# Optimization experiments

Measured on AMD Instinct MI355X. Metric: run time of the kernel, lower is better.

The kernel has to match this reference:

```python
import jax, jax.numpy as jnp
import numpy as np

H = 128
EPS = 1e-5

def _lstm_layer(x, Wih, Whh, bih, bhh):
    # x: [B,T,D] -> h_seq: [B,T,H]. PyTorch gate order: i,f,g,o.
    xw = jnp.einsum('btd,gd->btg', x, Wih) + bih + bhh  # [B,T,4H]
    B = x.shape[0]
    h0 = jnp.zeros((B, H), x.dtype)
    c0 = jnp.zeros((B, H), x.dtype)
    def step(carry, xt):
        h, c = carry
        gates = xt + h @ Whh.T  # [B,4H]
        i, f, g, o = jnp.split(gates, 4, axis=-1)
        i = jax.nn.sigmoid(i); f = jax.nn.sigmoid(f)
        g = jnp.tanh(g); o = jax.nn.sigmoid(o)
        c = f * c + i * g
        h = o * jnp.tanh(c)
        return (h, c), h
    _, hs = jax.lax.scan(step, (h0, c0), jnp.swapaxes(xw, 0, 1))  # [T,B,H]
    return jnp.swapaxes(hs, 0, 1)

def setup_inputs() -> dict:
    key = jax.random.key(0)
    ks = jax.random.split(key, 16)
    B, T, D = 1024, 512, 14
    s = 1.0 / np.sqrt(H)
    u = lambda k, shp: jax.random.uniform(k, shp, jnp.float32, -s, s)
    return {
        'x': jax.random.normal(ks[0], (B, T, D), jnp.float32),
        'Wih0': u(ks[1], (4 * H, D)), 'Whh0': u(ks[2], (4 * H, H)),
        'bih0': u(ks[3], (4 * H,)), 'bhh0': u(ks[4], (4 * H,)),
        'Wih1': u(ks[5], (4 * H, H)), 'Whh1': u(ks[6], (4 * H, H)),
        'bih1': u(ks[7], (4 * H,)), 'bhh1': u(ks[8], (4 * H,)),
        'gamma': jnp.ones((H,), jnp.float32), 'beta': jnp.zeros((H,), jnp.float32),
        'W1': u(ks[9], (32, H)), 'b1': u(ks[10], (32,)),
        'W2': u(ks[11], (1, 32)), 'b2': u(ks[12], (1,)),
    }

def reference(x, Wih0, Whh0, bih0, bhh0, Wih1, Whh1, bih1, bhh1,
              gamma, beta, W1, b1, W2, b2):
    h1 = _lstm_layer(x, Wih0, Whh0, bih0, bhh0)   # [B,T,H] (inter-layer dropout off: eval)
    h2 = _lstm_layer(h1, Wih1, Whh1, bih1, bhh1)  # [B,T,H]
    last = h2[:, -1, :]                            # [B,H]
    mu = jnp.mean(last, axis=0)
    var = jnp.mean((last - mu) ** 2, axis=0)       # biased, matching torch BN
    normalized = (last - mu) / jnp.sqrt(var + EPS) * gamma + beta
    z = jax.nn.relu(normalized @ W1.T + b1)        # dropout identity in eval
    out = z @ W2.T + b2                            # [B,1]
    return out.squeeze(-1)
```

## Files before the change

kernel.cpp:

```cpp
#include <hip/hip_runtime.h>


#define B_ 1024
#define T_ 512
#define D_ 14
#define H_ 128
#define NB 4
#define NT 512

#define L2E 1.44269504088896f
#define L2E2 2.88539008177793f

typedef _Float16 f16;
typedef _Float16 half4 __attribute__((ext_vector_type(4)));
typedef _Float16 half8 __attribute__((ext_vector_type(8)));
typedef _Float16 f16x2 __attribute__((ext_vector_type(2)));
typedef float floatx4 __attribute__((ext_vector_type(4)));

__device__ __forceinline__ float sigmP(float y) {
    return __builtin_amdgcn_rcpf(1.0f + __builtin_amdgcn_exp2f(-y));
}
__device__ __forceinline__ float tanhP(float y) {
    return 1.0f - 2.0f * __builtin_amdgcn_rcpf(1.0f + __builtin_amdgcn_exp2f(y));
}
__device__ __forceinline__ float tanhC(float c) {
    return tanhP(c * L2E2);
}

__device__ __forceinline__ half8 ldfrag_s(const float* __restrict__ p, float s) {
    half8 r;
#pragma unroll
    for (int j = 0; j < 8; ++j) r[j] = (f16)(p[j] * s);
    return r;
}

#define MFMA(a, b, c) __builtin_amdgcn_mfma_f32_16x16x32_f16((a), (b), (c), 0, 0, 0)

__global__ __launch_bounds__(NT, 2) void lstm_fused(
    const float* __restrict__ x,
    const float* __restrict__ Wih0, const float* __restrict__ Whh0,
    const float* __restrict__ bih0, const float* __restrict__ bhh0,
    const float* __restrict__ Wih1, const float* __restrict__ Whh1,
    const float* __restrict__ bih1, const float* __restrict__ bhh1,
    float* __restrict__ h2last)
{
    __shared__ __align__(16) f16 whh1lds[8][4][3][64][8];
    __shared__ __align__(16) f16 h1f[2][4][64][8];
    __shared__ __align__(16) f16 h2f[2][4][64][8];
    __shared__ __align__(16) f16 xf[2][64][8];

    const int tid = threadIdx.x;
    const int lane = tid & 63;
    const int wv = tid >> 6;
    const int n = lane & 15;
    const int q = lane >> 4;
    const int b0 = blockIdx.x * NB;

    {
        unsigned int* z1 = (unsigned int*)h1f;
        unsigned int* z2 = (unsigned int*)h2f;
#pragma unroll
        for (int i = 0; i < 4; ++i) {
            z1[tid + i * 512] = 0u;
            z2[tid + i * 512] = 0u;
        }
        ((unsigned int*)xf)[tid] = 0u;
    }
    __syncthreads();

    if (tid < NB) {
        xf[0][tid + 16][7] = (f16)1.0f;
        xf[1][tid + 16][7] = (f16)1.0f;
    }
    if (tid < 64) {
        int nn = tid & 15, kq = tid >> 4;
        if (nn < NB && kq < 2) {
            half8 v;
#pragma unroll
            for (int e = 0; e < 8; ++e) {
                int k = kq * 8 + e;
                v[e] = (k < D_) ? (f16)x[(size_t)(b0 + nn) * T_ * D_ + k]
                                : (k == 15 ? (f16)1.0f : (f16)0.0f);
            }
            *(half8*)&xf[0][tid][0] = v;
        }
    }

    const float* xpp = x + (size_t)(b0 + (tid & 3)) * T_ * D_ + D_ + (tid >> 2);

    if (wv < 4) {
        half8 aWhh0[2][4][4], aWih0[2][4];
#pragma unroll
        for (int jj = 0; jj < 2; ++jj) {
            const int wg = 2 * wv + jj;
#pragma unroll
            for (int g = 0; g < 4; ++g) {
                const float gs = (g == 2) ? L2E2 : L2E;
                const int gr = g * 128 + wg * 16 + n;
#pragma unroll
                for (int kt = 0; kt < 4; ++kt)
                    aWhh0[jj][g][kt] = ldfrag_s(Whh0 + (size_t)gr * H_ + kt * 32 + q * 8, gs);
                half8 w0;
#pragma unroll
                for (int e = 0; e < 8; ++e) {
                    int k = q * 8 + e;
                    if (k < D_)       w0[e] = (f16)(Wih0[(size_t)gr * D_ + k] * gs);
                    else if (k == 15) w0[e] = (f16)((bih0[gr] + bhh0[gr]) * gs);
                    else              w0[e] = (f16)0.0f;
                }
                aWih0[jj][g] = w0;
            }
        }
        floatx4 c1[2] = {{0.f, 0.f, 0.f, 0.f}, {0.f, 0.f, 0.f, 0.f}};
        __syncthreads();

        for (int p = 0; p <= T_; ++p) {
            const int cur = p & 1, nxt = cur ^ 1;
            if (p < T_) {
                float xp = 0.0f;
                if (tid < NB * D_ && (p + 1) < T_) xp = *xpp;

                floatx4 C0[2][4];
#pragma unroll
                for (int jj = 0; jj < 2; ++jj)
#pragma unroll
                    for (int g = 0; g < 4; ++g) C0[jj][g] = floatx4{0.f, 0.f, 0.f, 0.f};
                {
                    half8 bx = *(const half8*)&xf[cur][lane][0];
#pragma unroll
                    for (int jj = 0; jj < 2; ++jj)
#pragma unroll
                        for (int g = 0; g < 4; ++g) C0[jj][g] = MFMA(aWih0[jj][g], bx, C0[jj][g]);
                }
#pragma unroll
                for (int kt = 0; kt < 4; ++kt) {
                    half8 bh = *(const half8*)&h1f[cur][kt][lane][0];
#pragma unroll
                    for (int jj = 0; jj < 2; ++jj)
#pragma unroll
                        for (int g = 0; g < 4; ++g) C0[jj][g] = MFMA(aWhh0[jj][g][kt], bh, C0[jj][g]);
                }
#pragma unroll
                for (int jj = 0; jj < 2; ++jj) {
                    half4 hp;
#pragma unroll
                    for (int r = 0; r < 4; ++r) {
                        float i_ = sigmP(C0[jj][0][r]);
                        float f_ = sigmP(C0[jj][1][r]);
                        float g_ = tanhP(C0[jj][2][r]);
                        float o_ = sigmP(C0[jj][3][r]);
                        c1[jj][r] = f_ * c1[jj][r] + i_ * g_;
                        hp[r] = (f16)(o_ * tanhC(c1[jj][r]));
                    }
                    const int wg = 2 * wv + jj;
                    const int ktw = wg >> 1;
                    const int qw = (wg & 1) * 2 + (q >> 1);
                    const int eb = (q & 1) * 4;
                    if (n < NB) *(half4*)&h1f[nxt][ktw][n + 16 * qw][eb] = hp;
                }
                if (tid < NB * D_ && (p + 1) < T_) {
                    int k = tid >> 2;
                    xf[nxt][(tid & 3) + 16 * (k >> 3)][k & 7] = (f16)xp;
                    xpp += D_;
                }
            }
            __syncthreads();
        }
    } else {
        const int w = wv - 4;
        half8 aWih1[2][4][4], aWhh1k0[2][4];
        f16x2 b1p[2][4][2];
#pragma unroll
        for (int jj = 0; jj < 2; ++jj) {
            const int wg = 2 * w + jj;
#pragma unroll
            for (int g = 0; g < 4; ++g) {
                const float gs = (g == 2) ? L2E2 : L2E;
                const int gr = g * 128 + wg * 16 + n;
#pragma unroll
                for (int kt = 0; kt < 4; ++kt) {
                    aWih1[jj][g][kt] = ldfrag_s(Wih1 + (size_t)gr * H_ + kt * 32 + q * 8, gs);
                    half8 wf = ldfrag_s(Whh1 + (size_t)gr * H_ + kt * 32 + q * 8, gs);
                    if (kt == 0) aWhh1k0[jj][g] = wf;
                    else         *(half8*)&whh1lds[wg][g][kt - 1][lane][0] = wf;
                }
                const int gb = g * 128 + wg * 16 + q * 4;
                f16x2 p0, p1;
                p0[0] = (f16)((bih1[gb]     + bhh1[gb])     * gs);
                p0[1] = (f16)((bih1[gb + 1] + bhh1[gb + 1]) * gs);
                p1[0] = (f16)((bih1[gb + 2] + bhh1[gb + 2]) * gs);
                p1[1] = (f16)((bih1[gb + 3] + bhh1[gb + 3]) * gs);
                b1p[jj][g][0] = p0;
                b1p[jj][g][1] = p1;
            }
        }
        floatx4 c2[2] = {{0.f, 0.f, 0.f, 0.f}, {0.f, 0.f, 0.f, 0.f}};
        __syncthreads();

        for (int p = 0; p <= T_; ++p) {
            const int cur = p & 1, nxt = cur ^ 1;
            if (p >= 1) {
                floatx4 C1[2][4];
#pragma unroll
                for (int jj = 0; jj < 2; ++jj)
#pragma unroll
                    for (int g = 0; g < 4; ++g) C1[jj][g] = floatx4{0.f, 0.f, 0.f, 0.f};
#pragma unroll
                for (int kt = 0; kt < 4; ++kt) {
                    half8 bh = *(const half8*)&h1f[cur][kt][lane][0];
#pragma unroll
                    for (int jj = 0; jj < 2; ++jj)
#pragma unroll
                        for (int g = 0; g < 4; ++g) C1[jj][g] = MFMA(aWih1[jj][g][kt], bh, C1[jj][g]);
                }
                {
                    half8 bh = *(const half8*)&h2f[cur][0][lane][0];
#pragma unroll
                    for (int jj = 0; jj < 2; ++jj)
#pragma unroll
                        for (int g = 0; g < 4; ++g) C1[jj][g] = MFMA(aWhh1k0[jj][g], bh, C1[jj][g]);
                }
#pragma unroll
                for (int kt = 1; kt < 4; ++kt) {
                    half8 bh = *(const half8*)&h2f[cur][kt][lane][0];
#pragma unroll
                    for (int jj = 0; jj < 2; ++jj) {
                        const int wg = 2 * w + jj;
#pragma unroll
                        for (int g = 0; g < 4; ++g) {
                            half8 aw = *(const half8*)&whh1lds[wg][g][kt - 1][lane][0];
                            C1[jj][g] = MFMA(aw, bh, C1[jj][g]);
                        }
                    }
                }
#pragma unroll
                for (int jj = 0; jj < 2; ++jj) {
                    half4 hp;
                    floatx4 hv;
#pragma unroll
                    for (int r = 0; r < 4; ++r) {
                        float pi = C1[jj][0][r] + (float)b1p[jj][0][r >> 1][r & 1];
                        float pf = C1[jj][1][r] + (float)b1p[jj][1][r >> 1][r & 1];
                        float pg = C1[jj][2][r] + (float)b1p[jj][2][r >> 1][r & 1];
                        float po = C1[jj][3][r] + (float)b1p[jj][3][r >> 1][r & 1];
                        float i_ = sigmP(pi), f_ = sigmP(pf), g_ = tanhP(pg), o_ = sigmP(po);
                        c2[jj][r] = f_ * c2[jj][r] + i_ * g_;
                        hv[r] = o_ * tanhC(c2[jj][r]);
                        hp[r] = (f16)hv[r];
                    }
                    const int wg = 2 * w + jj;
                    const int ktw = wg >> 1;
                    const int qw = (wg & 1) * 2 + (q >> 1);
                    const int eb = (q & 1) * 4;
                    if (n < NB) {
                        *(half4*)&h2f[nxt][ktw][n + 16 * qw][eb] = hp;
                        if (p == T_) {
#pragma unroll
                            for (int r = 0; r < 4; ++r)
                                h2last[(size_t)(b0 + n) * H_ + wg * 16 + q * 4 + r] = hv[r];
                        }
                    }
                }
            }
            __syncthreads();
        }
    }
}

__global__ void bn_stats(const float* __restrict__ h2last, float* __restrict__ stats)
{
    __shared__ float red[2][8][128];
    const int tid = threadIdx.x;
    const int j = tid & 127, bs = tid >> 7;
    float s = 0.0f, ss = 0.0f;
    for (int bb = 0; bb < 128; ++bb) {
        float v = h2last[(size_t)(bb * 8 + bs) * H_ + j];
        s += v;
        ss += v * v;
    }
    red[0][bs][j] = s;
    red[1][bs][j] = ss;
    __syncthreads();
    if (tid < 128) {
        float S = 0.0f, SS = 0.0f;
#pragma unroll
        for (int k = 0; k < 8; ++k) { S += red[0][k][tid]; SS += red[1][k][tid]; }
        float mu = S * (1.0f / 1024.0f);
        float var = SS * (1.0f / 1024.0f) - mu * mu;
        stats[tid] = mu;
        stats[128 + tid] = __builtin_amdgcn_rsqf(var + 1e-5f);
    }
}

__global__ void bn_mlp(const float* __restrict__ h2last, const float* __restrict__ stats,
                       const float* __restrict__ gamma, const float* __restrict__ beta,
                       const float* __restrict__ W1, const float* __restrict__ b1,
                       const float* __restrict__ W2, const float* __restrict__ b2,
                       float* __restrict__ out)
{
    __shared__ float W1T[128][33];
    __shared__ float mus[128], isds[128], gs[128], bts[128], w2s[32];
    const int tid = threadIdx.x;
    const int b = blockIdx.x * 128 + tid;

    for (int i = tid; i < 4096; i += 128) {
        int k = i >> 7, j = i & 127;
        W1T[j][k] = W1[i];
    }
    mus[tid] = stats[tid];
    isds[tid] = stats[128 + tid];
    gs[tid] = gamma[tid];
    bts[tid] = beta[tid];
    if (tid < 32) w2s[tid] = W2[tid];
    __syncthreads();

    float z[32];
#pragma unroll
    for (int k = 0; k < 32; ++k) z[k] = b1[k];

    for (int j = 0; j < 128; ++j) {
        float nv = (h2last[(size_t)b * H_ + j] - mus[j]) * isds[j] * gs[j] + bts[j];
#pragma unroll
        for (int k = 0; k < 32; ++k) z[k] += W1T[j][k] * nv;
    }
    float o = b2[0];
#pragma unroll
    for (int k = 0; k < 32; ++k) o += w2s[k] * fmaxf(z[k], 0.0f);
    out[b] = o;
}

extern "C" void kernel_launch(void* const* d_in, const int* in_sizes, int n_in,
                              void* d_out, int out_size, void* d_ws, size_t ws_size,
                              hipStream_t stream)
{
    const float* x    = (const float*)d_in[0];
    const float* Wih0 = (const float*)d_in[1];
    const float* Whh0 = (const float*)d_in[2];
    const float* bih0 = (const float*)d_in[3];
    const float* bhh0 = (const float*)d_in[4];
    const float* Wih1 = (const float*)d_in[5];
    const float* Whh1 = (const float*)d_in[6];
    const float* bih1 = (const float*)d_in[7];
    const float* bhh1 = (const float*)d_in[8];
    const float* gamma = (const float*)d_in[9];
    const float* beta  = (const float*)d_in[10];
    const float* W1 = (const float*)d_in[11];
    const float* b1 = (const float*)d_in[12];
    const float* W2 = (const float*)d_in[13];
    const float* b2 = (const float*)d_in[14];

    float* h2last = (float*)d_ws;
    float* stats  = h2last + (size_t)B_ * H_;
    float* out = (float*)d_out;

    hipLaunchKernelGGL(lstm_fused, dim3(B_ / NB), dim3(NT), 0, stream,
                       x, Wih0, Whh0, bih0, bhh0, Wih1, Whh1, bih1, bhh1, h2last);
    hipLaunchKernelGGL(bn_stats, dim3(1), dim3(1024), 0, stream, h2last, stats);
    hipLaunchKernelGGL(bn_mlp, dim3(8), dim3(128), 0, stream,
                       h2last, stats, gamma, beta, W1, b1, W2, b2, out);
}
```

Before: 1.117 ms.

## Unify layer-0/layer-1 warps per gate tile and fuse LSTM cell math

Replaces the split where waves 0-3 ran layer 0 and waves 4-7 ran layer 1, each owning two gate tiles. Now every wave owns one 16-row gate tile of both layers and runs both layer steps, so each h1 fragment read from shared memory feeds both layers' MFMAs. More Whh1 fragments stay in registers and the LDS copy shrinks. The cell update is rewritten as one fused routine with five exp2 and two reciprocals in place of separate sigmoid and tanh calls. The cost is higher register pressure per wave, and the changed reciprocal algebra may lose some accuracy.

```diff
diff --git a/kernel.cpp b/kernel.cpp
--- a/kernel.cpp
+++ b/kernel.cpp
@@ -17,16 +17,6 @@
 typedef _Float16 f16x2 __attribute__((ext_vector_type(2)));
 typedef float floatx4 __attribute__((ext_vector_type(4)));
 
-__device__ __forceinline__ float sigmP(float y) {
-    return __builtin_amdgcn_rcpf(1.0f + __builtin_amdgcn_exp2f(-y));
-}
-__device__ __forceinline__ float tanhP(float y) {
-    return 1.0f - 2.0f * __builtin_amdgcn_rcpf(1.0f + __builtin_amdgcn_exp2f(y));
-}
-__device__ __forceinline__ float tanhC(float c) {
-    return tanhP(c * L2E2);
-}
-
 __device__ __forceinline__ half8 ldfrag_s(const float* __restrict__ p, float s) {
     half8 r;
 #pragma unroll
@@ -35,6 +25,24 @@
 }
 
 #define MFMA(a, b, c) __builtin_amdgcn_mfma_f32_16x16x32_f16((a), (b), (c), 0, 0, 0)
+
+__device__ __forceinline__ float cellP(float pi, float pf, float pg, float po, float& cs)
+{
+    float a = __builtin_amdgcn_exp2f(-pi);
+    float u = __builtin_amdgcn_exp2f(-pf);
+    float b = __builtin_amdgcn_exp2f(pg);
+    float d = __builtin_amdgcn_exp2f(-po);
+    float t1 = 1.0f + a;
+    float t3 = 1.0f + u;
+    float t2 = __builtin_fmaf(t1, b, t1);
+    float bm = b - 1.0f;
+    float num = __builtin_fmaf(L2E2 * bm, t3, cs * t2);
+    cs = num * __builtin_amdgcn_rcpf(t2 * t3);
+    float e = __builtin_amdgcn_exp2f(cs);
+    float t4 = 1.0f + d;
+    float t5 = __builtin_fmaf(t4, e, t4);
+    return (e - 1.0f) * __builtin_amdgcn_rcpf(t5);
+}
 
 __global__ __launch_bounds__(NT, 2) void lstm_fused(
     const float* __restrict__ x,
@@ -44,7 +52,7 @@
     const float* __restrict__ bih1, const float* __restrict__ bhh1,
     float* __restrict__ h2last)
 {
-    __shared__ __align__(16) f16 whh1lds[8][4][3][64][8];
+    __shared__ __align__(16) f16 whh1lds[8][4][2][64][8];
     __shared__ __align__(16) f16 h1f[2][4][64][8];
     __shared__ __align__(16) f16 h2f[2][4][64][8];
     __shared__ __align__(16) f16 xf[2][64][8];
@@ -88,182 +96,139 @@
 
     const float* xpp = x + (size_t)(b0 + (tid & 3)) * T_ * D_ + D_ + (tid >> 2);
 
-    if (wv < 4) {
-        half8 aWhh0[2][4][4], aWih0[2][4];
-#pragma unroll
-        for (int jj = 0; jj < 2; ++jj) {
-            const int wg = 2 * wv + jj;
-#pragma unroll
-            for (int g = 0; g < 4; ++g) {
-                const float gs = (g == 2) ? L2E2 : L2E;
-                const int gr = g * 128 + wg * 16 + n;
-#pragma unroll
-                for (int kt = 0; kt < 4; ++kt)
-                    aWhh0[jj][g][kt] = ldfrag_s(Whh0 + (size_t)gr * H_ + kt * 32 + q * 8, gs);
-                half8 w0;
-#pragma unroll
-                for (int e = 0; e < 8; ++e) {
-                    int k = q * 8 + e;
-                    if (k < D_)       w0[e] = (f16)(Wih0[(size_t)gr * D_ + k] * gs);
-                    else if (k == 15) w0[e] = (f16)((bih0[gr] + bhh0[gr]) * gs);
-                    else              w0[e] = (f16)0.0f;
+    const int wg = wv;
+    half8 aWhh0[4][4], aWih0[4];
+    half8 aWih1[4][4], aWhh1r[4][2];
+    f16x2 b1p[4][2];
+#pragma unroll
+    for (int g = 0; g < 4; ++g) {
+        const float gs = (g == 2) ? L2E2 : L2E;
+        const int gr = g * 128 + wg * 16 + n;
+#pragma unroll
+        for (int kt = 0; kt < 4; ++kt)
+            aWhh0[g][kt] = ldfrag_s(Whh0 + (size_t)gr * H_ + kt * 32 + q * 8, gs);
+        half8 w0;
+#pragma unroll
+        for (int e = 0; e < 8; ++e) {
+            int k = q * 8 + e;
+            if (k < D_)       w0[e] = (f16)(Wih0[(size_t)gr * D_ + k] * gs);
+            else if (k == 15) w0[e] = (f16)((bih0[gr] + bhh0[gr]) * gs);
+            else              w0[e] = (f16)0.0f;
+        }
+        aWih0[g] = w0;
+#pragma unroll
+        for (int kt = 0; kt < 4; ++kt) {
+            aWih1[g][kt] = ldfrag_s(Wih1 + (size_t)gr * H_ + kt * 32 + q * 8, gs);
+            half8 wf = ldfrag_s(Whh1 + (size_t)gr * H_ + kt * 32 + q * 8, gs);
+            if (kt < 2) aWhh1r[g][kt] = wf;
+            else        *(half8*)&whh1lds[wg][g][kt - 2][lane][0] = wf;
+        }
+        const int gb = g * 128 + wg * 16 + q * 4;
+        f16x2 p0, p1;
+        p0[0] = (f16)((bih1[gb]     + bhh1[gb])     * gs);
+        p0[1] = (f16)((bih1[gb + 1] + bhh1[gb + 1]) * gs);
+        p1[0] = (f16)((bih1[gb + 2] + bhh1[gb + 2]) * gs);
+        p1[1] = (f16)((bih1[gb + 3] + bhh1[gb + 3]) * gs);
+        b1p[g][0] = p0;
+        b1p[g][1] = p1;
+    }
+
+    floatx4 cs1 = {0.f, 0.f, 0.f, 0.f};
+    floatx4 cs2 = {0.f, 0.f, 0.f, 0.f};
+    __syncthreads();
+
+    for (int p = 0; p <= T_; ++p) {
+        const int cur = p & 1, nxt = cur ^ 1;
+        const bool doA = (p < T_);
+        const bool doB = (p >= 1);
+
+        float xp = 0.0f;
+        if (tid < NB * D_ && (p + 1) < T_) xp = *xpp;
+
+        floatx4 C0[4], C1[4];
+#pragma unroll
+        for (int g = 0; g < 4; ++g) {
+            C0[g] = floatx4{0.f, 0.f, 0.f, 0.f};
+            C1[g] = floatx4{0.f, 0.f, 0.f, 0.f};
+        }
+
+        if (doA) {
+            half8 bx = *(const half8*)&xf[cur][lane][0];
+#pragma unroll
+            for (int g = 0; g < 4; ++g) C0[g] = MFMA(aWih0[g], bx, C0[g]);
+        }
+#pragma unroll
+        for (int kt = 0; kt < 4; ++kt) {
+            half8 bh = *(const half8*)&h1f[cur][kt][lane][0];
+            if (doA) {
+#pragma unroll
+                for (int g = 0; g < 4; ++g) C0[g] = MFMA(aWhh0[g][kt], bh, C0[g]);
+            }
+            if (doB) {
+#pragma unroll
+                for (int g = 0; g < 4; ++g) C1[g] = MFMA(aWih1[g][kt], bh, C1[g]);
+            }
+        }
+        if (doB) {
+#pragma unroll
+            for (int kt = 0; kt < 2; ++kt) {
+                half8 bh = *(const half8*)&h2f[cur][kt][lane][0];
+#pragma unroll
+                for (int g = 0; g < 4; ++g) C1[g] = MFMA(aWhh1r[g][kt], bh, C1[g]);
+            }
+#pragma unroll
+            for (int kt = 2; kt < 4; ++kt) {
+                half8 bh = *(const half8*)&h2f[cur][kt][lane][0];
+#pragma unroll
+                for (int g = 0; g < 4; ++g) {
+                    half8 aw = *(const half8*)&whh1lds[wg][g][kt - 2][lane][0];
+                    C1[g] = MFMA(aw, bh, C1[g]);
                 }
-                aWih0[jj][g] = w0;
-            }
-        }
-        floatx4 c1[2] = {{0.f, 0.f, 0.f, 0.f}, {0.f, 0.f, 0.f, 0.f}};
+            }
+        }
+
+        const int ktw = wg >> 1;
+        const int qw = (wg & 1) * 2 + (q >> 1);
+        const int eb = (q & 1) * 4;
+        if (doA) {
+            half4 hp;
+#pragma unroll
+            for (int r = 0; r < 4; ++r) {
+                float c = cs1[r];
+                hp[r] = (f16)cellP(C0[0][r], C0[1][r], C0[2][r], C0[3][r], c);
+                cs1[r] = c;
+            }
+            if (n < NB) *(half4*)&h1f[nxt][ktw][n + 16 * qw][eb] = hp;
+        }
+        if (doB) {
+            half4 hp;
+            floatx4 hv;
+#pragma unroll
+            for (int r = 0; r < 4; ++r) {
+                float pi = C1[0][r] + (float)b1p[0][r >> 1][r & 1];
+                float pf = C1[1][r] + (float)b1p[1][r >> 1][r & 1];
+                float pg = C1[2][r] + (float)b1p[2][r >> 1][r & 1];
+                float po = C1[3][r] + (float)b1p[3][r >> 1][r & 1];
+                float c = cs2[r];
+                hv[r] = cellP(pi, pf, pg, po, c);
+                cs2[r] = c;
+                hp[r] = (f16)hv[r];
+            }
+            if (n < NB) {
+                *(half4*)&h2f[nxt][ktw][n + 16 * qw][eb] = hp;
+                if (p == T_) {
+#pragma unroll
+                    for (int r = 0; r < 4; ++r)
+                        h2last[(size_t)(b0 + n) * H_ + wg * 16 + q * 4 + r] = hv[r];
+                }
+            }
+        }
+        if (tid < NB * D_ && (p + 1) < T_) {
+            int k = tid >> 2;
+            xf[nxt][(tid & 3) + 16 * (k >> 3)][k & 7] = (f16)xp;
+            xpp += D_;
+        }
         __syncthreads();
-
-        for (int p = 0; p <= T_; ++p) {
-            const int cur = p & 1, nxt = cur ^ 1;
-            if (p < T_) {
-                float xp = 0.0f;
-                if (tid < NB * D_ && (p + 1) < T_) xp = *xpp;
-
-                floatx4 C0[2][4];
-#pragma unroll
-                for (int jj = 0; jj < 2; ++jj)
-#pragma unroll
-                    for (int g = 0; g < 4; ++g) C0[jj][g] = floatx4{0.f, 0.f, 0.f, 0.f};
-                {
-                    half8 bx = *(const half8*)&xf[cur][lane][0];
-#pragma unroll
-                    for (int jj = 0; jj < 2; ++jj)
-#pragma unroll
-                        for (int g = 0; g < 4; ++g) C0[jj][g] = MFMA(aWih0[jj][g], bx, C0[jj][g]);
-                }
-#pragma unroll
-                for (int kt = 0; kt < 4; ++kt) {
-                    half8 bh = *(const half8*)&h1f[cur][kt][lane][0];
-#pragma unroll
-                    for (int jj = 0; jj < 2; ++jj)
-#pragma unroll
-                        for (int g = 0; g < 4; ++g) C0[jj][g] = MFMA(aWhh0[jj][g][kt], bh, C0[jj][g]);
-                }
-#pragma unroll
-                for (int jj = 0; jj < 2; ++jj) {
-                    half4 hp;
-#pragma unroll
-                    for (int r = 0; r < 4; ++r) {
-                        float i_ = sigmP(C0[jj][0][r]);
-                        float f_ = sigmP(C0[jj][1][r]);
-                        float g_ = tanhP(C0[jj][2][r]);
-                        float o_ = sigmP(C0[jj][3][r]);
-                        c1[jj][r] = f_ * c1[jj][r] + i_ * g_;
-                        hp[r] = (f16)(o_ * tanhC(c1[jj][r]));
-                    }
-                    const int wg = 2 * wv + jj;
-                    const int ktw = wg >> 1;
-                    const int qw = (wg & 1) * 2 + (q >> 1);
-                    const int eb = (q & 1) * 4;
-                    if (n < NB) *(half4*)&h1f[nxt][ktw][n + 16 * qw][eb] = hp;
-                }
-                if (tid < NB * D_ && (p + 1) < T_) {
-                    int k = tid >> 2;
-                    xf[nxt][(tid & 3) + 16 * (k >> 3)][k & 7] = (f16)xp;
-                    xpp += D_;
-                }
-            }
-            __syncthreads();
-        }
-    } else {
-        const int w = wv - 4;
-        half8 aWih1[2][4][4], aWhh1k0[2][4];
-        f16x2 b1p[2][4][2];
-#pragma unroll
-        for (int jj = 0; jj < 2; ++jj) {
-            const int wg = 2 * w + jj;
-#pragma unroll
-            for (int g = 0; g < 4; ++g) {
-                const float gs = (g == 2) ? L2E2 : L2E;
-                const int gr = g * 128 + wg * 16 + n;
-#pragma unroll
-                for (int kt = 0; kt < 4; ++kt) {
-                    aWih1[jj][g][kt] = ldfrag_s(Wih1 + (size_t)gr * H_ + kt * 32 + q * 8, gs);
-                    half8 wf = ldfrag_s(Whh1 + (size_t)gr * H_ + kt * 32 + q * 8, gs);
-                    if (kt == 0) aWhh1k0[jj][g] = wf;
-                    else         *(half8*)&whh1lds[wg][g][kt - 1][lane][0] = wf;
-                }
-                const int gb = g * 128 + wg * 16 + q * 4;
-                f16x2 p0, p1;
-                p0[0] = (f16)((bih1[gb]     + bhh1[gb])     * gs);
-                p0[1] = (f16)((bih1[gb + 1] + bhh1[gb + 1]) * gs);
-                p1[0] = (f16)((bih1[gb + 2] + bhh1[gb + 2]) * gs);
-                p1[1] = (f16)((bih1[gb + 3] + bhh1[gb + 3]) * gs);
-                b1p[jj][g][0] = p0;
-                b1p[jj][g][1] = p1;
-            }
-        }
-        floatx4 c2[2] = {{0.f, 0.f, 0.f, 0.f}, {0.f, 0.f, 0.f, 0.f}};
-        __syncthreads();
-
-        for (int p = 0; p <= T_; ++p) {
-            const int cur = p & 1, nxt = cur ^ 1;
-            if (p >= 1) {
-                floatx4 C1[2][4];
-#pragma unroll
-                for (int jj = 0; jj < 2; ++jj)
-#pragma unroll
-                    for (int g = 0; g < 4; ++g) C1[jj][g] = floatx4{0.f, 0.f, 0.f, 0.f};
-#pragma unroll
-                for (int kt = 0; kt < 4; ++kt) {
-                    half8 bh = *(const half8*)&h1f[cur][kt][lane][0];
-#pragma unroll
-                    for (int jj = 0; jj < 2; ++jj)
-#pragma unroll
-                        for (int g = 0; g < 4; ++g) C1[jj][g] = MFMA(aWih1[jj][g][kt], bh, C1[jj][g]);
-                }
-                {
-                    half8 bh = *(const half8*)&h2f[cur][0][lane][0];
-#pragma unroll
-                    for (int jj = 0; jj < 2; ++jj)
-#pragma unroll
-                        for (int g = 0; g < 4; ++g) C1[jj][g] = MFMA(aWhh1k0[jj][g], bh, C1[jj][g]);
-                }
-#pragma unroll
-                for (int kt = 1; kt < 4; ++kt) {
-                    half8 bh = *(const half8*)&h2f[cur][kt][lane][0];
-#pragma unroll
-                    for (int jj = 0; jj < 2; ++jj) {
-                        const int wg = 2 * w + jj;
-#pragma unroll
-                        for (int g = 0; g < 4; ++g) {
-                            half8 aw = *(const half8*)&whh1lds[wg][g][kt - 1][lane][0];
-                            C1[jj][g] = MFMA(aw, bh, C1[jj][g]);
-                        }
-                    }
-                }
-#pragma unroll
-                for (int jj = 0; jj < 2; ++jj) {
-                    half4 hp;
-                    floatx4 hv;
-#pragma unroll
-                    for (int r = 0; r < 4; ++r) {
-                        float pi = C1[jj][0][r] + (float)b1p[jj][0][r >> 1][r & 1];
-                        float pf = C1[jj][1][r] + (float)b1p[jj][1][r >> 1][r & 1];
-                        float pg = C1[jj][2][r] + (float)b1p[jj][2][r >> 1][r & 1];
-                        float po = C1[jj][3][r] + (float)b1p[jj][3][r >> 1][r & 1];
-                        float i_ = sigmP(pi), f_ = sigmP(pf), g_ = tanhP(pg), o_ = sigmP(po);
-                        c2[jj][r] = f_ * c2[jj][r] + i_ * g_;
-                        hv[r] = o_ * tanhC(c2[jj][r]);
-                        hp[r] = (f16)hv[r];
-                    }
-                    const int wg = 2 * w + jj;
-                    const int ktw = wg >> 1;
-                    const int qw = (wg & 1) * 2 + (q >> 1);
-                    const int eb = (q & 1) * 4;
-                    if (n < NB) {
-                        *(half4*)&h2f[nxt][ktw][n + 16 * qw][eb] = hp;
-                        if (p == T_) {
-#pragma unroll
-                            for (int r = 0; r < 4; ++r)
-                                h2last[(size_t)(b0 + n) * H_ + wg * 16 + q * 4 + r] = hv[r];
-                        }
-                    }
-                }
-            }
-            __syncthreads();
-        }
     }
 }
 
```

After: 1.081 ms. 1.03x faster.
